# Optimization experiments

Measured on AMD Instinct MI355X. Metric: run time of the kernel, lower is better.

The kernel has to match this reference:

```python
import jax, jax.numpy as jnp
import numpy as np

GWIDTH2 = 0.3  # Gaussian bandwidth squared
PNORM = 2


def setup_inputs() -> dict:
    key = jax.random.key(0)
    k1, k2 = jax.random.split(key)
    b, c, h, w = 16, 3, 256, 256
    npro = 32
    x = jax.random.uniform(k1, (b, c, h, w), dtype=jnp.float32)  # pixel values in [0,1]
    P = jax.random.uniform(k2, (npro, c), dtype=jnp.float32)     # p x c prototype pixels
    return {"x": x, "P": P}


def reference(x, P):
    # x: (b, c, h, w); P: (p, c)
    b, c, h, w = x.shape
    # broadcast difference -> (b, p, c, h, w); pnorm=2 distance over channels
    diff = x[:, None, :, :, :] - P[None, :, :, None, None]
    normsp = jnp.sum(diff ** PNORM, axis=2) ** (1.0 / PNORM)  # (b, p, h, w)
    expo = jnp.exp(-normsp / (2.0 * GWIDTH2))
    Y = jnp.sum(expo, axis=(2, 3))  # (b, p)
    return Y / (h * w)
```

## Files before the change

### kernel.cpp

```cpp
#include <hip/hip_runtime.h>


#define NPRO    32
#define HW      65536
#define THREADS 256
#define BPB     32
#define POISON  0xAAAAAAAAu

typedef float v2f __attribute__((ext_vector_type(2)));

__global__ __launch_bounds__(THREADS) void soft_count_kernel(
    const float* __restrict__ x, const float* __restrict__ P,
    float* __restrict__ out)
{
    __shared__ float sP[NPRO * 3];
    __shared__ float sred[4][NPRO];

    const float A = 2.4044917f;

    const int tid = threadIdx.x;
    if (tid < NPRO * 3) sP[tid] = P[tid] * A;
    __syncthreads();

    const int b   = blockIdx.x / BPB;
    const int blk = blockIdx.x % BPB;

    const float* base = x + (size_t)b * 3 * HW;

    v2f r2[4], g2[4], b2[4];
#pragma unroll
    for (int k = 0; k < 2; ++k) {
        const int idx = blk * (THREADS * 8) + k * (THREADS * 4) + tid * 4;
        const float4 r4 = *(const float4*)(base + idx);
        const float4 g4 = *(const float4*)(base + HW + idx);
        const float4 b4 = *(const float4*)(base + 2 * HW + idx);
        r2[k*2+0] = (v2f){r4.x * A, r4.y * A};
        r2[k*2+1] = (v2f){r4.z * A, r4.w * A};
        g2[k*2+0] = (v2f){g4.x * A, g4.y * A};
        g2[k*2+1] = (v2f){g4.z * A, g4.w * A};
        b2[k*2+0] = (v2f){b4.x * A, b4.y * A};
        b2[k*2+1] = (v2f){b4.z * A, b4.w * A};
    }

    float acc[NPRO];
#pragma unroll
    for (int p = 0; p < NPRO; ++p) {
        const float p0 = sP[p * 3 + 0];
        const float p1 = sP[p * 3 + 1];
        const float p2 = sP[p * 3 + 2];
        const v2f P0 = (v2f){p0, p0};
        const v2f P1 = (v2f){p1, p1};
        const v2f P2 = (v2f){p2, p2};
        float s = 0.0f;
#pragma unroll
        for (int j = 0; j < 4; ++j) {
            const v2f d0 = r2[j] - P0;
            const v2f d1 = g2[j] - P1;
            const v2f d2 = b2[j] - P2;
            v2f n2 = d0 * d0;
            n2 = __builtin_elementwise_fma(d1, d1, n2);
            n2 = __builtin_elementwise_fma(d2, d2, n2);
            s += __builtin_amdgcn_exp2f(-__builtin_amdgcn_sqrtf(n2.x));
            s += __builtin_amdgcn_exp2f(-__builtin_amdgcn_sqrtf(n2.y));
        }
        acc[p] = s;
    }

    const int lane = tid & 63;
    const int wv   = tid >> 6;
#pragma unroll
    for (int p = 0; p < NPRO; ++p) {
        float v = acc[p];
#pragma unroll
        for (int off = 32; off >= 1; off >>= 1)
            v += __shfl_down(v, off, 64);
        if (lane == 0) sred[wv][p] = v;
    }
    __syncthreads();

    if (tid < NPRO) {
        const float v = (sred[0][tid] + sred[1][tid] + sred[2][tid] + sred[3][tid])
                        * (1.0f / (float)HW);
        float* addr = &out[b * NPRO + tid];
        const unsigned int old =
            atomicCAS((unsigned int*)addr, POISON, __float_as_uint(v));
        if (old != POISON) atomicAdd(addr, v);
    }
}

extern "C" void kernel_launch(void* const* d_in, const int* in_sizes, int n_in,
                              void* d_out, int out_size, void* d_ws, size_t ws_size,
                              hipStream_t stream) {
    const float* x = (const float*)d_in[0];
    const float* P = (const float*)d_in[1];
    float* out = (float*)d_out;

    const int nb = in_sizes[0] / (3 * HW);

    soft_count_kernel<<<nb * BPB, THREADS, 0, stream>>>(x, P, out);
}
```

Measured before the change: 74.75 us.

## Halve per-thread pixels, double blocks, fuse scaling into FMA, pack reductions

Each thread now handles 4 pixels instead of 8, and blocks per batch double from 32 to 64, so there are twice as many blocks and fewer registers per thread. Occupancy is raised through a launch_bounds hint. The pixel scaling is folded into an FMA with negated, pre-scaled prototypes, which removes the separate multiply and subtract. Reduction accumulators are packed into float2 and reduced with xor shuffles so two values are added per packed op. The cost is twice as many blocks doing the shuffle reduction and atomic tail, which shifts the balance toward reduction overhead.

After: 75.14 us. About the same (+0.5%).

```diff
diff --git a/kernel.cpp b/kernel.cpp
--- a/kernel.cpp
+++ b/kernel.cpp
@@ -4,77 +4,77 @@
 #define NPRO    32
 #define HW      65536
 #define THREADS 256
-#define BPB     32
+#define BPB     64
 #define POISON  0xAAAAAAAAu
 
 typedef float v2f __attribute__((ext_vector_type(2)));
 
-__global__ __launch_bounds__(THREADS) void soft_count_kernel(
+__global__ __launch_bounds__(THREADS, 4) void soft_count_kernel(
     const float* __restrict__ x, const float* __restrict__ P,
     float* __restrict__ out)
 {
-    __shared__ float sP[NPRO * 3];
+    __shared__ float sPn[NPRO * 3];
     __shared__ float sred[4][NPRO];
 
     const float A = 2.4044917f;
 
     const int tid = threadIdx.x;
-    if (tid < NPRO * 3) sP[tid] = P[tid] * A;
+    if (tid < NPRO * 3) sPn[tid] = P[tid] * (-A);
     __syncthreads();
 
     const int b   = blockIdx.x / BPB;
     const int blk = blockIdx.x % BPB;
 
     const float* base = x + (size_t)b * 3 * HW;
+    const int idx = blk * (THREADS * 4) + tid * 4;
 
-    v2f r2[4], g2[4], b2[4];
-#pragma unroll
-    for (int k = 0; k < 2; ++k) {
-        const int idx = blk * (THREADS * 8) + k * (THREADS * 4) + tid * 4;
-        const float4 r4 = *(const float4*)(base + idx);
-        const float4 g4 = *(const float4*)(base + HW + idx);
-        const float4 b4 = *(const float4*)(base + 2 * HW + idx);
-        r2[k*2+0] = (v2f){r4.x * A, r4.y * A};
-        r2[k*2+1] = (v2f){r4.z * A, r4.w * A};
-        g2[k*2+0] = (v2f){g4.x * A, g4.y * A};
-        g2[k*2+1] = (v2f){g4.z * A, g4.w * A};
-        b2[k*2+0] = (v2f){b4.x * A, b4.y * A};
-        b2[k*2+1] = (v2f){b4.z * A, b4.w * A};
-    }
+    const float4 r4 = *(const float4*)(base + idx);
+    const float4 g4 = *(const float4*)(base + HW + idx);
+    const float4 b4 = *(const float4*)(base + 2 * HW + idx);
 
-    float acc[NPRO];
+    const v2f Av = (v2f){A, A};
+    v2f r2[2] = { (v2f){r4.x, r4.y}, (v2f){r4.z, r4.w} };
+    v2f g2[2] = { (v2f){g4.x, g4.y}, (v2f){g4.z, g4.w} };
+    v2f b2[2] = { (v2f){b4.x, b4.y}, (v2f){b4.z, b4.w} };
+
+    v2f acc2[NPRO / 2];
 #pragma unroll
     for (int p = 0; p < NPRO; ++p) {
-        const float p0 = sP[p * 3 + 0];
-        const float p1 = sP[p * 3 + 1];
-        const float p2 = sP[p * 3 + 2];
-        const v2f P0 = (v2f){p0, p0};
-        const v2f P1 = (v2f){p1, p1};
-        const v2f P2 = (v2f){p2, p2};
+        const float q0 = sPn[p * 3 + 0];
+        const float q1 = sPn[p * 3 + 1];
+        const float q2 = sPn[p * 3 + 2];
+        const v2f P0 = (v2f){q0, q0};
+        const v2f P1 = (v2f){q1, q1};
+        const v2f P2 = (v2f){q2, q2};
         float s = 0.0f;
 #pragma unroll
-        for (int j = 0; j < 4; ++j) {
-            const v2f d0 = r2[j] - P0;
-            const v2f d1 = g2[j] - P1;
-            const v2f d2 = b2[j] - P2;
+        for (int j = 0; j < 2; ++j) {
+            const v2f d0 = __builtin_elementwise_fma(r2[j], Av, P0);
+            const v2f d1 = __builtin_elementwise_fma(g2[j], Av, P1);
+            const v2f d2 = __builtin_elementwise_fma(b2[j], Av, P2);
             v2f n2 = d0 * d0;
             n2 = __builtin_elementwise_fma(d1, d1, n2);
             n2 = __builtin_elementwise_fma(d2, d2, n2);
             s += __builtin_amdgcn_exp2f(-__builtin_amdgcn_sqrtf(n2.x));
             s += __builtin_amdgcn_exp2f(-__builtin_amdgcn_sqrtf(n2.y));
         }
-        acc[p] = s;
+        if (p & 1) acc2[p >> 1].y = s;
+        else       acc2[p >> 1].x = s;
     }
 
     const int lane = tid & 63;
     const int wv   = tid >> 6;
 #pragma unroll
-    for (int p = 0; p < NPRO; ++p) {
-        float v = acc[p];
+    for (int q = 0; q < NPRO / 2; ++q) {
+        v2f v = acc2[q];
 #pragma unroll
-        for (int off = 32; off >= 1; off >>= 1)
-            v += __shfl_down(v, off, 64);
-        if (lane == 0) sred[wv][p] = v;
+        for (int off = 32; off >= 1; off >>= 1) {
+            v2f o;
+            o.x = __shfl_xor(v.x, off, 64);
+            o.y = __shfl_xor(v.y, off, 64);
+            v += o;
+        }
+        if (lane == 0) { sred[wv][2 * q] = v.x; sred[wv][2 * q + 1] = v.y; }
     }
     __syncthreads();
 
```
